# Kernel optimization log

Hardware: AMD Instinct MI355X
Metric: run time of the kernel (lower is better)

The kernel has to match this reference:

```python
import jax, jax.numpy as jnp
import numpy as np
from jax import lax

DIM, D_INNER, D_STATE, D_CONV, DT_RANK = 256, 512, 16, 4, 16
B_, H_, W_ = 4, 64, 64


def setup_inputs() -> dict:
    key = jax.random.key(0)
    ks = jax.random.split(key, 10)
    s = lambda k, shape, scale: (jax.random.normal(k, shape, dtype=jnp.float32) * scale)
    inp = {
        "x": s(ks[0], (B_, DIM, H_, W_), 1.0),
        "in_proj_w": s(ks[1], (2 * D_INNER, DIM), DIM ** -0.5),
        "conv_w": s(ks[2], (D_INNER, 1, D_CONV), D_CONV ** -0.5),
        "conv_b": s(ks[3], (D_INNER,), 0.02),
        "x_proj_w": s(ks[4], (DT_RANK + 2 * D_STATE, D_INNER), D_INNER ** -0.5),
        "dt_proj_w": s(ks[5], (D_INNER, DT_RANK), DT_RANK ** -0.5),
        "dt_proj_b": s(ks[6], (D_INNER,), 0.02),
        # A_log init: log(arange(1..d_state)) broadcast over channels (standard S4D-real init)
        "A_log": jnp.broadcast_to(jnp.log(jnp.arange(1, D_STATE + 1, dtype=jnp.float32)), (D_INNER, D_STATE)).copy(),
        "D": jnp.ones((D_INNER,), dtype=jnp.float32),
        "out_proj_w": s(ks[7], (DIM, D_INNER), D_INNER ** -0.5),
    }
    return inp


def _mamba_forward(x, in_proj_w, conv_w, conv_b, x_proj_w, dt_proj_w, dt_proj_b, A_log, D, out_proj_w):
    b, c, h, w = x.shape
    L = h * w
    xs = x.reshape(b, c, L).transpose(0, 2, 1)                      # [b, L, dim]

    xz = jnp.einsum('bld,ed->ble', xs, in_proj_w)                   # [b, L, 2*d_inner]
    u, res = jnp.split(xz, 2, axis=-1)                              # each [b, L, d_inner]

    # causal depthwise conv1d over sequence
    u_t = u.transpose(0, 2, 1)                                      # [b, d_inner, L]
    u_t = lax.conv_general_dilated(u_t, conv_w, window_strides=(1,),
                                   padding=[(D_CONV - 1, 0)],
                                   feature_group_count=D_INNER,
                                   dimension_numbers=('NCH', 'OIH', 'NCH'))
    u = jax.nn.silu(u_t.transpose(0, 2, 1) + conv_b)                # [b, L, d_inner]

    dbc = jnp.einsum('bld,ed->ble', u, x_proj_w)                    # [b, L, dt_rank+2n]
    dt, Bm, Cm = jnp.split(dbc, [DT_RANK, DT_RANK + D_STATE], axis=-1)
    delta = jax.nn.softplus(jnp.einsum('blr,dr->bld', dt, dt_proj_w) + dt_proj_b)  # [b,L,d_inner]

    A = -jnp.exp(A_log)                                             # [d_inner, n]
    deltaA = jnp.exp(jnp.einsum('bld,dn->bldn', delta, A))          # [b,L,d,n]
    deltaBu = jnp.einsum('bld,bln,bld->bldn', delta, Bm, u)         # [b,L,d,n]

    def step(state, inp):
        dA, dBu, c_t = inp                                          # [b,d,n],[b,d,n],[b,n]
        state = dA * state + dBu
        y = jnp.einsum('bdn,bn->bd', state, c_t)
        return state, y

    init = jnp.zeros((b, D_INNER, D_STATE), dtype=x.dtype)
    _, ys = lax.scan(step, init, (jnp.moveaxis(deltaA, 1, 0),
                                  jnp.moveaxis(deltaBu, 1, 0),
                                  jnp.moveaxis(Cm, 1, 0)))
    y = jnp.moveaxis(ys, 0, 1) + u * D                              # [b, L, d_inner]
    y = y * jax.nn.silu(res)
    out = jnp.einsum('ble,de->bld', y, out_proj_w)                  # [b, L, dim]
    return out.transpose(0, 2, 1).reshape(b, c, h, w)


def reference(x, in_proj_w, conv_w, conv_b, x_proj_w, dt_proj_w, dt_proj_b, A_log, D, out_proj_w):
    return _mamba_forward(x, in_proj_w, conv_w, conv_b, x_proj_w, dt_proj_w, dt_proj_b, A_log, D, out_proj_w)
```

## Files before the change

kernel.cpp:

```cpp
#include <hip/hip_runtime.h>
#include <math.h>


namespace {
constexpr int kB   = 4;
constexpr int kDim = 256;
constexpr int kL   = 4096;
constexpr int kDI  = 512;
constexpr int kN   = 16;
constexpr int kNC  = 128;
constexpr int kCS  = 32;
}

typedef __attribute__((ext_vector_type(8))) short bf16x8;
typedef __attribute__((ext_vector_type(4))) float f32x4;
typedef __attribute__((ext_vector_type(2))) float f32x2;

__device__ __forceinline__ float rcpf(float x) { return __builtin_amdgcn_rcpf(x); }
__device__ __forceinline__ float siluf(float x) { return x * rcpf(1.f + __expf(-x)); }
__device__ __forceinline__ float softplusf(float x) {
  return fmaxf(x, 0.f) + __logf(1.f + __expf(-fabsf(x)));
}

__device__ __forceinline__ unsigned short f2bf(float x) {
  union { float f; unsigned int u; } v; v.f = x;
  unsigned int u = v.u;
  u += 0x7fffu + ((u >> 16) & 1u);
  return (unsigned short)(u >> 16);
}
__device__ __forceinline__ float bf2f(unsigned short u) {
  union { unsigned int i; float f; } v; v.i = ((unsigned int)u) << 16; return v.f;
}

__device__ __forceinline__ void gload_lds16(const void* g, void* l) {
  __builtin_amdgcn_global_load_lds(
      (const __attribute__((address_space(1))) unsigned int*)g,
      (__attribute__((address_space(3))) unsigned int*)l, 16, 0, 0);
}

__global__ __launch_bounds__(256) void k_prep(const float* __restrict__ w_in,
                                              const float* __restrict__ w_out,
                                              const float* __restrict__ w_x,
                                              const float* __restrict__ w_dt,
                                              const float* __restrict__ A_log,
                                              const float* __restrict__ x,
                                              unsigned short* __restrict__ wib,
                                              unsigned short* __restrict__ wob,
                                              unsigned short* __restrict__ wxb,
                                              unsigned short* __restrict__ wdtb,
                                              float* __restrict__ Avz,
                                              unsigned int* __restrict__ flagA,
                                              unsigned short* __restrict__ xt) {
  __shared__ float Xs[64][65];
  const int blk = blockIdx.x;
  const int t = threadIdx.x;
  if (blk < 1760) {
    int idx = blk * 256 + t;
    if (idx < 262144) wib[idx] = f2bf(w_in[idx]);
    else if (idx < 393216) wob[idx - 262144] = f2bf(w_out[idx - 262144]);
    else if (idx < 417792) wxb[idx - 393216] = f2bf(w_x[idx - 393216]);
    else {
      int i = idx - 417792;
      int r = i & 31, d = i >> 5;
      wdtb[i] = (r < 16) ? f2bf(w_dt[d * 16 + r]) : (unsigned short)0;
    }
  } else if (blk < 1762) {
    int d = (blk - 1760) * 256 + t;
    float a0 = -__expf(A_log[d * kN]);
    bool ok = true;
#pragma unroll
    for (int n = 1; n < kN; ++n) {
      float av = -__expf(A_log[d * kN + n]);
      ok = ok && (fabsf(av - (n + 1) * a0) <= 1e-5f * fabsf(av));
    }
    Avz[d] = a0;
    unsigned long long bal = __ballot(ok);
    int wv = t >> 6;
    if ((t & 63) == 0) ((unsigned long long*)Xs)[wv] = bal;
    __syncthreads();
    if (t == 0) {
      unsigned long long all = ~0ull;
#pragma unroll
      for (int w = 0; w < 4; ++w) all &= ((unsigned long long*)Xs)[w];
      flagA[blk - 1760] = (all == ~0ull) ? 1u : 0u;
    }
  } else {
    int id = blk - 1762;
    int lb = id & 63, db = (id >> 6) & 3, b = id >> 8;
    const int d0 = db * 64, l0 = lb * 64, l = t & 63;
#pragma unroll
    for (int rep = 0; rep < 16; ++rep) {
      int dd = rep * 4 + (t >> 6);
      Xs[dd][l] = x[((size_t)b * kDim + d0 + dd) * kL + l0 + l];
    }
    __syncthreads();
#pragma unroll
    for (int rep = 0; rep < 8; ++rep) {
      int lj = rep * 8 + (t >> 5);
      int di = (t & 31) * 2;
      ushort2 v;
      v.x = f2bf(Xs[di][lj]);
      v.y = f2bf(Xs[di + 1][lj]);
      *(ushort2*)(xt + ((size_t)b * kL + l0 + lj) * kDim + d0 + di) = v;
    }
  }
}

__global__ __launch_bounds__(256) void gemm_in_lm(const unsigned short* __restrict__ xt,
                                                  const unsigned short* __restrict__ W,
                                                  unsigned short* __restrict__ ubf,
                                                  unsigned short* __restrict__ resb) {
  __shared__ __align__(16) unsigned short As[128 * 64];
  __shared__ __align__(16) unsigned short Bs[128 * 64];
  const int e0 = blockIdx.x * 128;
  const int l0 = blockIdx.y * 128;
  const int b  = blockIdx.z;
  const int t  = threadIdx.x;
  const int wave = t >> 6, lane = t & 63;
  const int wm = wave >> 1, wn = wave & 1;
  const unsigned short* Ab = xt + (size_t)b * kL * kDim;

  f32x4 acc[4][4];
#pragma unroll
  for (int i = 0; i < 4; ++i)
#pragma unroll
    for (int j = 0; j < 4; ++j) acc[i][j] = (f32x4)0.0f;

  const int srow = t >> 3, sch = t & 7;
  for (int kt = 0; kt < 4; ++kt) {
    const int k0 = kt * 64;
#pragma unroll
    for (int c = 0; c < 4; ++c) {
      int row = c * 32 + srow;
      int gch = sch ^ (row & 7);
      gload_lds16(Ab + (size_t)(l0 + row) * kDim + k0 + gch * 8,
                  (char*)As + c * 4096 + wave * 1024);
      gload_lds16(W  + (size_t)(e0 + row) * kDim + k0 + gch * 8,
                  (char*)Bs + c * 4096 + wave * 1024);
    }
    __syncthreads();
#pragma unroll
    for (int ks = 0; ks < 2; ++ks) {
      bf16x8 af[4], bfr[4];
#pragma unroll
      for (int f = 0; f < 4; ++f) {
        int ra = wm * 64 + f * 16 + (lane & 15);
        int ca = (ks * 4 + (lane >> 4)) ^ (ra & 7);
        af[f] = *(const bf16x8*)((const char*)As + ra * 128 + ca * 16);
        int rb = wn * 64 + f * 16 + (lane & 15);
        int cb = (ks * 4 + (lane >> 4)) ^ (rb & 7);
        bfr[f] = *(const bf16x8*)((const char*)Bs + rb * 128 + cb * 16);
      }
#pragma unroll
      for (int i = 0; i < 4; ++i)
#pragma unroll
        for (int j = 0; j < 4; ++j)
          acc[i][j] = __builtin_amdgcn_mfma_f32_16x16x32_bf16(af[i], bfr[j], acc[i][j], 0, 0, 0);
    }
    __syncthreads();
  }

  const bool is_u = (e0 < kDI);
  unsigned short* dst = is_u ? ubf : resb;
  const int ebase = is_u ? e0 : (e0 - kDI);
#pragma unroll
  for (int i = 0; i < 4; ++i)
#pragma unroll
    for (int j = 0; j < 4; ++j)
#pragma unroll
      for (int r = 0; r < 4; ++r) {
        int l = l0 + wm * 64 + i * 16 + (lane >> 4) * 4 + r;
        int e = ebase + wn * 64 + j * 16 + (lane & 15);
        dst[((size_t)b * kL + l) * kDI + e] = f2bf(acc[i][j][r]);
      }
}

__global__ __launch_bounds__(256) void k_conv(const unsigned short* __restrict__ ubf,
                                              const float* __restrict__ cw,
                                              const float* __restrict__ cb,
                                              unsigned short* __restrict__ ucb) {
  int idx = blockIdx.x * 256 + threadIdx.x;
  int d8 = idx & 63;
  int l  = (idx >> 6) & (kL - 1);
  int b  = idx >> 18;
  int d0 = d8 * 8;
  const unsigned short* row = ubf + ((size_t)b * kL + l) * kDI + d0;
  uint4 zero = make_uint4(0, 0, 0, 0);
  uint4 c0 = *(const uint4*)row;
  uint4 c1 = (l >= 1) ? *(const uint4*)(row - kDI)     : zero;
  uint4 c2 = (l >= 2) ? *(const uint4*)(row - 2 * kDI) : zero;
  uint4 c3 = (l >= 3) ? *(const uint4*)(row - 3 * kDI) : zero;
  const unsigned int* p0 = (const unsigned int*)&c0;
  const unsigned int* p1 = (const unsigned int*)&c1;
  const unsigned int* p2 = (const unsigned int*)&c2;
  const unsigned int* p3 = (const unsigned int*)&c3;
  unsigned short ov[8];
#pragma unroll
  for (int c = 0; c < 8; ++c) {
    int q = c >> 1, hi = c & 1;
    float u0 = bf2f((unsigned short)(hi ? (p0[q] >> 16) : (p0[q] & 0xffff)));
    float u1 = bf2f((unsigned short)(hi ? (p1[q] >> 16) : (p1[q] & 0xffff)));
    float u2 = bf2f((unsigned short)(hi ? (p2[q] >> 16) : (p2[q] & 0xffff)));
    float u3 = bf2f((unsigned short)(hi ? (p3[q] >> 16) : (p3[q] & 0xffff)));
    float4 w = *(const float4*)(cw + (d0 + c) * 4);
    float acc = cb[d0 + c] + w.x * u3 + w.y * u2 + w.z * u1 + w.w * u0;
    ov[c] = f2bf(siluf(acc));
  }
  *(uint4*)(ucb + ((size_t)b * kL + l) * kDI + d0) = *(const uint4*)ov;
}

__global__ __launch_bounds__(256) void k_xproj_dt(const unsigned short* __restrict__ Wx,
                                                  const unsigned short* __restrict__ Wdtb,
                                                  const float* __restrict__ bdt,
                                                  float* __restrict__ dbcBC,
                                                  const unsigned short* __restrict__ ucb,
                                                  unsigned short* __restrict__ delb) {
  __shared__ __align__(16) unsigned short As[64 * 64];
  __shared__ __align__(16) unsigned short Bs[128 * 64];
  __shared__ __align__(16) unsigned short dtTl[128 * 32];
  __shared__ __align__(16) unsigned short Wl[128 * 32];
  const int l0 = blockIdx.x * 128;
  const int b  = blockIdx.y;
  const int t  = threadIdx.x;
  const int wave = t >> 6, lane = t & 63;
  const unsigned short* Bb = ucb + (size_t)b * kL * kDI;

  f32x4 acc[3][2];
#pragma unroll
  for (int i = 0; i < 3; ++i)
#pragma unroll
    for (int j = 0; j < 2; ++j) acc[i][j] = (f32x4)0.0f;

  const int srow = t >> 3, sch = t & 7;
  for (int kt = 0; kt < 8; ++kt) {
    const int k0 = kt * 64;
#pragma unroll
    for (int c = 0; c < 2; ++c) {
      int row = c * 32 + srow;
      int grow = row < 48 ? row : 47;
      int gch = sch ^ (row & 7);
      gload_lds16(Wx + (size_t)grow * kDI + k0 + gch * 8,
                  (char*)As + c * 4096 + wave * 1024);
    }
#pragma unroll
    for (int c = 0; c < 4; ++c) {
      int row = c * 32 + srow;
      int gch = sch ^ (row & 7);
      gload_lds16(Bb + (size_t)(l0 + row) * kDI + k0 + gch * 8,
                  (char*)Bs + c * 4096 + wave * 1024);
    }
    __syncthreads();
#pragma unroll
    for (int ks = 0; ks < 2; ++ks) {
      bf16x8 af[3], bfr[2];
#pragma unroll
      for (int f = 0; f < 3; ++f) {
        int ra = f * 16 + (lane & 15);
        int ca = (ks * 4 + (lane >> 4)) ^ (ra & 7);
        af[f] = *(const bf16x8*)((const char*)As + ra * 128 + ca * 16);
      }
#pragma unroll
      for (int f = 0; f < 2; ++f) {
        int rb = wave * 32 + f * 16 + (lane & 15);
        int cb = (ks * 4 + (lane >> 4)) ^ (rb & 7);
        bfr[f] = *(const bf16x8*)((const char*)Bs + rb * 128 + cb * 16);
      }
#pragma unroll
      for (int i = 0; i < 3; ++i)
#pragma unroll
        for (int j = 0; j < 2; ++j)
          acc[i][j] = __builtin_amdgcn_mfma_f32_16x16x32_bf16(af[i], bfr[j], acc[i][j], 0, 0, 0);
    }
    __syncthreads();
  }

#pragma unroll
  for (int i = 1; i < 3; ++i)
#pragma unroll
    for (int j = 0; j < 2; ++j)
#pragma unroll
      for (int r = 0; r < 4; ++r) {
        int m = i * 16 + (lane >> 4) * 4 + r;
        int l = l0 + wave * 32 + j * 16 + (lane & 15);
        dbcBC[((size_t)b * 32 + (m - 16)) * kL + l] = acc[i][j][r];
      }
#pragma unroll
  for (int j = 0; j < 2; ++j) {
    int l = wave * 32 + j * 16 + (lane & 15);
    int m0 = (lane >> 4) * 4;
    ushort4 v;
    v.x = f2bf(acc[0][j][0]); v.y = f2bf(acc[0][j][1]);
    v.z = f2bf(acc[0][j][2]); v.w = f2bf(acc[0][j][3]);
    int byte = l * 64 + (((m0 >> 3) ^ (l & 3)) << 4) + ((m0 & 7) << 1);
    *(ushort4*)((char*)dtTl + byte) = v;
  }
  {
    int lz = t >> 1, zc = 2 + (t & 1);
    *(uint4*)((char*)dtTl + lz * 64 + ((zc ^ (lz & 3)) << 4)) = make_uint4(0, 0, 0, 0);
  }
  __syncthreads();

  const int wl = wave >> 1, wd = wave & 1;
  for (int dt4 = 0; dt4 < 4; ++dt4) {
#pragma unroll
    for (int c2 = 0; c2 < 2; ++c2) {
      int unit = c2 * 256 + t;
      int row = unit >> 2, sc = unit & 3;
      int gch = sc ^ (row & 3);
      gload_lds16(Wdtb + (size_t)(dt4 * 128 + row) * 32 + gch * 8,
                  (char*)Wl + c2 * 4096 + t * 16);
    }
    __syncthreads();
    f32x4 acc2[4][4];
#pragma unroll
    for (int i = 0; i < 4; ++i)
#pragma unroll
      for (int j = 0; j < 4; ++j) acc2[i][j] = (f32x4)0.0f;
    bf16x8 afr[4], bfr2[4];
#pragma unroll
    for (int f = 0; f < 4; ++f) {
      int ra = wl * 64 + f * 16 + (lane & 15);
      afr[f] = *(const bf16x8*)((const char*)dtTl + ra * 64 + (((lane >> 4) ^ (ra & 3)) << 4));
      int rb = wd * 64 + f * 16 + (lane & 15);
      bfr2[f] = *(const bf16x8*)((const char*)Wl + rb * 64 + (((lane >> 4) ^ (rb & 3)) << 4));
    }
#pragma unroll
    for (int i = 0; i < 4; ++i)
#pragma unroll
      for (int j = 0; j < 4; ++j)
        acc2[i][j] = __builtin_amdgcn_mfma_f32_16x16x32_bf16(afr[i], bfr2[j], acc2[i][j], 0, 0, 0);
#pragma unroll
    for (int j = 0; j < 4; ++j) {
      int d = dt4 * 128 + wd * 64 + j * 16 + (lane & 15);
      float bd = bdt[d];
#pragma unroll
      for (int i = 0; i < 4; ++i)
#pragma unroll
        for (int r = 0; r < 4; ++r) {
          int l = l0 + wl * 64 + i * 16 + (lane >> 4) * 4 + r;
          float delta = softplusf(acc2[i][j][r] + bd);
          delb[((size_t)b * kL + l) * kDI + d] = f2bf(delta);
        }
    }
    __syncthreads();
  }
}

__global__ __launch_bounds__(256) void k_scanA(const unsigned short* __restrict__ delb,
                                               const unsigned short* __restrict__ ucb,
                                               const float* __restrict__ dbcBC,
                                               const float* __restrict__ A_log,
                                               const float* __restrict__ Avz,
                                               const unsigned int* __restrict__ flagA,
                                               float* __restrict__ P,
                                               float* __restrict__ S) {
  __shared__ __align__(16) float Bsh[16][kCS];
  const int b = blockIdx.z, ch = blockIdx.y;
  const int t = threadIdx.x;
  const int d = blockIdx.x * 256 + t;
  const int l0 = ch * kCS;
  {
    int row = t >> 4, li = (t & 15) * 2;
    *(float2*)&Bsh[row][li] =
        *(const float2*)&dbcBC[((size_t)b * 32 + row) * kL + l0 + li];
  }
  __syncthreads();
  const bool fast = (flagA[0] != 0u) && (flagA[1] != 0u);
  const float Av0 = Avz[d];
  const unsigned short* pDel = delb + ((size_t)b * kL + l0) * kDI + d;
  const unsigned short* pU = ucb + ((size_t)b * kL + l0) * kDI + d;
  size_t obase = (size_t)(b * kNC + ch) * (kN * kDI) + d;

  if (fast) {
    f32x2 Sv2[8];
#pragma unroll
    for (int m = 0; m < 8; ++m) Sv2[m] = (f32x2){0.f, 0.f};
    float Pprod = 1.f;
    for (int i = 0; i < kCS; i += 4) {
      f32x2 a2[4], e2[4], du2[4];
#pragma unroll
      for (int jj = 0; jj < 4; ++jj) {
        float dl = bf2f(pDel[(size_t)(i + jj) * kDI]);
        float uu = bf2f(pU[(size_t)(i + jj) * kDI]);
        float E = __expf(dl * Av0);
        float duv = dl * uu;
        du2[jj] = (f32x2){duv, duv};
        float Esq = E * E;
        a2[jj] = (f32x2){E, Esq};
        e2[jj] = (f32x2){Esq, Esq};
        Pprod *= E;
      }
#pragma unroll
      for (int m = 0; m < 8; ++m) {
        float4 Ba = *(const float4*)&Bsh[2 * m][i];
        float4 Bb = *(const float4*)&Bsh[2 * m + 1][i];
        Sv2[m] = Sv2[m] * a2[0] + du2[0] * (f32x2){Ba.x, Bb.x};
        Sv2[m] = Sv2[m] * a2[1] + du2[1] * (f32x2){Ba.y, Bb.y};
        Sv2[m] = Sv2[m] * a2[2] + du2[2] * (f32x2){Ba.z, Bb.z};
        Sv2[m] = Sv2[m] * a2[3] + du2[3] * (f32x2){Ba.w, Bb.w};
        if (m < 7) {
          a2[0] *= e2[0]; a2[1] *= e2[1]; a2[2] *= e2[2]; a2[3] *= e2[3];
        }
      }
    }
    float pw = Pprod;
#pragma unroll
    for (int n = 0; n < kN; ++n) {
      P[obase + (size_t)n * kDI] = pw;
      S[obase + (size_t)n * kDI] = (n & 1) ? Sv2[n >> 1].y : Sv2[n >> 1].x;
      pw *= Pprod;
    }
  } else {
    float Av[16];
#pragma unroll
    for (int n = 0; n < kN; ++n) Av[n] = -__expf(A_log[d * kN + n]);
    float Pv[16], Sv[16];
#pragma unroll
    for (int n = 0; n < kN; ++n) { Pv[n] = 1.f; Sv[n] = 0.f; }
    for (int i = 0; i < kCS; i += 4) {
      float del[4], du[4];
#pragma unroll
      for (int jj = 0; jj < 4; ++jj) {
        del[jj] = bf2f(pDel[(size_t)(i + jj) * kDI]);
        du[jj] = del[jj] * bf2f(pU[(size_t)(i + jj) * kDI]);
      }
#pragma unroll
      for (int n = 0; n < kN; ++n) {
        float4 B4 = *(const float4*)&Bsh[n][i];
        float a;
        a = __expf(del[0] * Av[n]); Pv[n] *= a; Sv[n] = Sv[n] * a + du[0] * B4.x;
        a = __expf(del[1] * Av[n]); Pv[n] *= a; Sv[n] = Sv[n] * a + du[1] * B4.y;
        a = __expf(del[2] * Av[n]); Pv[n] *= a; Sv[n] = Sv[n] * a + du[2] * B4.z;
        a = __expf(del[3] * Av[n]); Pv[n] *= a; Sv[n] = Sv[n] * a + du[3] * B4.w;
      }
    }
#pragma unroll
    for (int n = 0; n < kN; ++n) {
      P[obase + (size_t)n * kDI] = Pv[n];
      S[obase + (size_t)n * kDI] = Sv[n];
    }
  }
}

__global__ __launch_bounds__(256) void k_scanB(const float* __restrict__ P,
                                               const float* __restrict__ S,
                                               float* __restrict__ init) {
  int idx = blockIdx.x * 256 + threadIdx.x;
  int b = idx >> 13, nd = idx & 8191;
  size_t base = (size_t)b * kNC * 8192 + nd;
  float carry = 0.f;
  for (int c0 = 0; c0 < kNC; c0 += 8) {
    float p[8], s[8];
#pragma unroll
    for (int j = 0; j < 8; ++j) {
      size_t o = base + (size_t)(c0 + j) * 8192;
      p[j] = P[o]; s[j] = S[o];
    }
#pragma unroll
    for (int j = 0; j < 8; ++j) {
      init[base + (size_t)(c0 + j) * 8192] = carry;
      carry = p[j] * carry + s[j];
    }
  }
}

__global__ __launch_bounds__(256) void k_scanC(const unsigned short* __restrict__ delb,
                                               const unsigned short* __restrict__ ucb,
                                               const float* __restrict__ dbcBC,
                                               const float* __restrict__ A_log,
                                               const float* __restrict__ Avz,
                                               const unsigned int* __restrict__ flagA,
                                               const float* __restrict__ init,
                                               const unsigned short* __restrict__ resb,
                                               const float* __restrict__ Dp,
                                               unsigned short* __restrict__ yt) {
  __shared__ __align__(16) float BCsh[32][kCS];
  const int b = blockIdx.z, ch = blockIdx.y;
  const int t = threadIdx.x;
  const int d = blockIdx.x * 256 + t;
  const int l0 = ch * kCS;
  {
    int row = t >> 3, li = (t & 7) * 4;
    *(float4*)&BCsh[row][li] =
        *(const float4*)&dbcBC[((size_t)b * 32 + row) * kL + l0 + li];
  }
  __syncthreads();
  const bool fast = (flagA[0] != 0u) && (flagA[1] != 0u);
  const float Av0 = Avz[d];
  const float Dv = Dp[d];
  const unsigned short* pDel = delb + ((size_t)b * kL + l0) * kDI + d;
  const unsigned short* pU = ucb + ((size_t)b * kL + l0) * kDI + d;
  const unsigned short* pR = resb + ((size_t)b * kL + l0) * kDI + d;
  unsigned short* pY = yt + ((size_t)b * kL + l0) * kDI + d;
  size_t ibase = (size_t)(b * kNC + ch) * (kN * kDI) + d;

  if (fast) {
    f32x2 s2[8];
#pragma unroll
    for (int m = 0; m < 8; ++m)
      s2[m] = (f32x2){init[ibase + (size_t)(2 * m) * kDI],
                      init[ibase + (size_t)(2 * m + 1) * kDI]};
    for (int i = 0; i < kCS; i += 4) {
      float uv[4];
      f32x2 a2[4], e2[4], du2[4], yacc2[4];
#pragma unroll
      for (int jj = 0; jj < 4; ++jj) {
        float dl = bf2f(pDel[(size_t)(i + jj) * kDI]);
        uv[jj] = bf2f(pU[(size_t)(i + jj) * kDI]);
        float E = __expf(dl * Av0);
        float duv = dl * uv[jj];
        du2[jj] = (f32x2){duv, duv};
        float Esq = E * E;
        a2[jj] = (f32x2){E, Esq};
        e2[jj] = (f32x2){Esq, Esq};
        yacc2[jj] = (f32x2){0.f, 0.f};
      }
#pragma unroll
      for (int m = 0; m < 8; ++m) {
        float4 Ba = *(const float4*)&BCsh[2 * m][i];
        float4 Bb = *(const float4*)&BCsh[2 * m + 1][i];
        float4 Ca = *(const float4*)&BCsh[16 + 2 * m][i];
        float4 Cb = *(const float4*)&BCsh[16 + 2 * m + 1][i];
        s2[m] = s2[m] * a2[0] + du2[0] * (f32x2){Ba.x, Bb.x};
        yacc2[0] = yacc2[0] + s2[m] * (f32x2){Ca.x, Cb.x};
        s2[m] = s2[m] * a2[1] + du2[1] * (f32x2){Ba.y, Bb.y};
        yacc2[1] = yacc2[1] + s2[m] * (f32x2){Ca.y, Cb.y};
        s2[m] = s2[m] * a2[2] + du2[2] * (f32x2){Ba.z, Bb.z};
        yacc2[2] = yacc2[2] + s2[m] * (f32x2){Ca.z, Cb.z};
        s2[m] = s2[m] * a2[3] + du2[3] * (f32x2){Ba.w, Bb.w};
        yacc2[3] = yacc2[3] + s2[m] * (f32x2){Ca.w, Cb.w};
        if (m < 7) {
          a2[0] *= e2[0]; a2[1] *= e2[1]; a2[2] *= e2[2]; a2[3] *= e2[3];
        }
      }
#pragma unroll
      for (int jj = 0; jj < 4; ++jj) {
        float yv = yacc2[jj].x + yacc2[jj].y;
        float r = bf2f(pR[(size_t)(i + jj) * kDI]);
        float gv = (yv + uv[jj] * Dv) * siluf(r);
        pY[(size_t)(i + jj) * kDI] = f2bf(gv);
      }
    }
  } else {
    float Av[16];
#pragma unroll
    for (int n = 0; n < kN; ++n) Av[n] = -__expf(A_log[d * kN + n]);
    float s[16];
#pragma unroll
    for (int n = 0; n < kN; ++n) s[n] = init[ibase + (size_t)n * kDI];
    for (int i = 0; i < kCS; i += 4) {
      float uv[4], du[4], del[4], yacc[4] = {0.f, 0.f, 0.f, 0.f};
#pragma unroll
      for (int jj = 0; jj < 4; ++jj) {
        del[jj] = bf2f(pDel[(size_t)(i + jj) * kDI]);
        uv[jj] = bf2f(pU[(size_t)(i + jj) * kDI]);
        du[jj] = del[jj] * uv[jj];
      }
#pragma unroll
      for (int n = 0; n < kN; ++n) {
        float4 B4 = *(const float4*)&BCsh[n][i];
        float4 C4 = *(const float4*)&BCsh[16 + n][i];
        float a;
        a = __expf(del[0] * Av[n]); s[n] = s[n] * a + du[0] * B4.x; yacc[0] += s[n] * C4.x;
        a = __expf(del[1] * Av[n]); s[n] = s[n] * a + du[1] * B4.y; yacc[1] += s[n] * C4.y;
        a = __expf(del[2] * Av[n]); s[n] = s[n] * a + du[2] * B4.z; yacc[2] += s[n] * C4.z;
        a = __expf(del[3] * Av[n]); s[n] = s[n] * a + du[3] * B4.w; yacc[3] += s[n] * C4.w;
      }
#pragma unroll
      for (int jj = 0; jj < 4; ++jj) {
        float r = bf2f(pR[(size_t)(i + jj) * kDI]);
        float gv = (yacc[jj] + uv[jj] * Dv) * siluf(r);
        pY[(size_t)(i + jj) * kDI] = f2bf(gv);
      }
    }
  }
}

__global__ __launch_bounds__(256) void gemm_out(const unsigned short* __restrict__ A,
                                                const unsigned short* __restrict__ Bt,
                                                float* __restrict__ C0) {
  __shared__ __align__(16) unsigned short As[128 * 64];
  __shared__ __align__(16) unsigned short Bs[128 * 64];
  const int n0 = blockIdx.x * 128;
  const int m0 = blockIdx.y * 128;
  const int b  = blockIdx.z;
  const int t  = threadIdx.x;
  const int wave = t >> 6, lane = t & 63;
  const int wm = wave >> 1, wn = wave & 1;
  const unsigned short* Bb = Bt + (size_t)b * kL * kDI;

  f32x4 acc[4][4];
#pragma unroll
  for (int i = 0; i < 4; ++i)
#pragma unroll
    for (int j = 0; j < 4; ++j) acc[i][j] = (f32x4)0.0f;

  const int srow = t >> 3, sch = t & 7;
  for (int kt = 0; kt < 8; ++kt) {
    const int k0 = kt * 64;
#pragma unroll
    for (int c = 0; c < 4; ++c) {
      int row = c * 32 + srow;
      int gch = sch ^ (row & 7);
      gload_lds16(A  + (size_t)(m0 + row) * kDI + k0 + gch * 8,
                  (char*)As + c * 4096 + wave * 1024);
      gload_lds16(Bb + (size_t)(n0 + row) * kDI + k0 + gch * 8,
                  (char*)Bs + c * 4096 + wave * 1024);
    }
    __syncthreads();
#pragma unroll
    for (int ks = 0; ks < 2; ++ks) {
      bf16x8 af[4], bfr[4];
#pragma unroll
      for (int f = 0; f < 4; ++f) {
        int ra = wm * 64 + f * 16 + (lane & 15);
        int ca = (ks * 4 + (lane >> 4)) ^ (ra & 7);
        af[f] = *(const bf16x8*)((const char*)As + ra * 128 + ca * 16);
        int rb = wn * 64 + f * 16 + (lane & 15);
        int cb = (ks * 4 + (lane >> 4)) ^ (rb & 7);
        bfr[f] = *(const bf16x8*)((const char*)Bs + rb * 128 + cb * 16);
      }
#pragma unroll
      for (int i = 0; i < 4; ++i)
#pragma unroll
        for (int j = 0; j < 4; ++j)
          acc[i][j] = __builtin_amdgcn_mfma_f32_16x16x32_bf16(af[i], bfr[j], acc[i][j], 0, 0, 0);
    }
    __syncthreads();
  }
#pragma unroll
  for (int i = 0; i < 4; ++i)
#pragma unroll
    for (int j = 0; j < 4; ++j)
#pragma unroll
      for (int r = 0; r < 4; ++r) {
        int m = m0 + wm * 64 + i * 16 + (lane >> 4) * 4 + r;
        int n = n0 + wn * 64 + j * 16 + (lane & 15);
        C0[((size_t)b * kDim + m) * kL + n] = acc[i][j][r];
      }
}

extern "C" void kernel_launch(void* const* d_in, const int* in_sizes, int n_in,
                              void* d_out, int out_size, void* d_ws, size_t ws_size,
                              hipStream_t stream) {
  const float* x       = (const float*)d_in[0];
  const float* in_w    = (const float*)d_in[1];
  const float* conv_w  = (const float*)d_in[2];
  const float* conv_b  = (const float*)d_in[3];
  const float* xproj_w = (const float*)d_in[4];
  const float* dt_w    = (const float*)d_in[5];
  const float* dt_b    = (const float*)d_in[6];
  const float* A_log   = (const float*)d_in[7];
  const float* Dp      = (const float*)d_in[8];
  const float* out_w   = (const float*)d_in[9];
  float* out = (float*)d_out;

  float* ws = (float*)d_ws;
  const size_t nBLD  = (size_t)kB * kL * kDI;
  const size_t nPS   = (size_t)kB * kNC * kN * kDI;
  float* dbcBC = ws;
  float* Pb    = dbcBC + 524288;
  float* Sb    = Pb + nPS;
  float* initb = Sb + nPS;
  unsigned short* ubf  = (unsigned short*)(initb + nPS);
  unsigned short* ucb  = ubf + nBLD;
  unsigned short* resb = ucb + nBLD;
  unsigned short* delb = resb + nBLD;
  unsigned short* wib  = delb + nBLD;
  unsigned short* wob  = wib + 262144;
  unsigned short* wxb  = wob + 131072;
  unsigned short* wdtb = wxb + 24576;
  float* Avz           = (float*)(wdtb + 32768);
  unsigned int* flagA  = (unsigned int*)(Avz + 512);
  unsigned short* xt   = delb;
  unsigned short* yt   = (unsigned short*)Pb;

  k_prep<<<dim3(2786), 256, 0, stream>>>(in_w, out_w, xproj_w, dt_w, A_log, x,
                                         wib, wob, wxb, wdtb, Avz, flagA, xt);
  gemm_in_lm<<<dim3(8, kL / 128, kB), 256, 0, stream>>>(xt, wib, ubf, resb);
  k_conv<<<dim3((unsigned)(kB * kL * 64 / 256)), 256, 0, stream>>>(ubf, conv_w, conv_b, ucb);
  k_xproj_dt<<<dim3(kL / 128, kB), 256, 0, stream>>>(wxb, wdtb, dt_b, dbcBC, ucb, delb);
  k_scanA<<<dim3(2, kNC, kB), 256, 0, stream>>>(delb, ucb, dbcBC, A_log, Avz, flagA, Pb, Sb);
  k_scanB<<<dim3(kB * kDI * kN / 256), 256, 0, stream>>>(Pb, Sb, initb);
  k_scanC<<<dim3(2, kNC, kB), 256, 0, stream>>>(delb, ucb, dbcBC, A_log, Avz, flagA, initb, resb, Dp, yt);
  gemm_out<<<dim3(kL / 128, kDim / 128, kB), 256, 0, stream>>>(wob, yt, out);
}
```

Measured before the change: 155.0 us.

## Store per-chunk decay product once and rebuild state powers in scanB

```diff
diff --git a/kernel.cpp b/kernel.cpp
--- a/kernel.cpp
+++ b/kernel.cpp
@@ -346,23 +346,24 @@
   }
 }
 
-__global__ __launch_bounds__(256) void k_scanA(const unsigned short* __restrict__ delb,
+__global__ __launch_bounds__(128) void k_scanA(const unsigned short* __restrict__ delb,
                                                const unsigned short* __restrict__ ucb,
                                                const float* __restrict__ dbcBC,
                                                const float* __restrict__ A_log,
                                                const float* __restrict__ Avz,
                                                const unsigned int* __restrict__ flagA,
-                                               float* __restrict__ P,
+                                               float* __restrict__ Pprod,
+                                               float* __restrict__ Pfull,
                                                float* __restrict__ S) {
   __shared__ __align__(16) float Bsh[16][kCS];
   const int b = blockIdx.z, ch = blockIdx.y;
   const int t = threadIdx.x;
-  const int d = blockIdx.x * 256 + t;
+  const int d = blockIdx.x * 128 + t;
   const int l0 = ch * kCS;
   {
-    int row = t >> 4, li = (t & 15) * 2;
-    *(float2*)&Bsh[row][li] =
-        *(const float2*)&dbcBC[((size_t)b * 32 + row) * kL + l0 + li];
+    int row = t >> 3, li = (t & 7) * 4;
+    *(float4*)&Bsh[row][li] =
+        *(const float4*)&dbcBC[((size_t)b * 32 + row) * kL + l0 + li];
   }
   __syncthreads();
   const bool fast = (flagA[0] != 0u) && (flagA[1] != 0u);
@@ -375,7 +376,7 @@
     f32x2 Sv2[8];
 #pragma unroll
     for (int m = 0; m < 8; ++m) Sv2[m] = (f32x2){0.f, 0.f};
-    float Pprod = 1.f;
+    float Pp = 1.f;
     for (int i = 0; i < kCS; i += 4) {
       f32x2 a2[4], e2[4], du2[4];
 #pragma unroll
@@ -388,7 +389,7 @@
         float Esq = E * E;
         a2[jj] = (f32x2){E, Esq};
         e2[jj] = (f32x2){Esq, Esq};
-        Pprod *= E;
+        Pp *= E;
       }
 #pragma unroll
       for (int m = 0; m < 8; ++m) {
@@ -403,13 +404,10 @@
         }
       }
     }
-    float pw = Pprod;
-#pragma unroll
-    for (int n = 0; n < kN; ++n) {
-      P[obase + (size_t)n * kDI] = pw;
+    Pprod[(size_t)(b * kNC + ch) * kDI + d] = Pp;
+#pragma unroll
+    for (int n = 0; n < kN; ++n)
       S[obase + (size_t)n * kDI] = (n & 1) ? Sv2[n >> 1].y : Sv2[n >> 1].x;
-      pw *= Pprod;
-    }
   } else {
     float Av[16];
 #pragma unroll
@@ -436,35 +434,65 @@
     }
 #pragma unroll
     for (int n = 0; n < kN; ++n) {
-      P[obase + (size_t)n * kDI] = Pv[n];
+      Pfull[obase + (size_t)n * kDI] = Pv[n];
       S[obase + (size_t)n * kDI] = Sv[n];
     }
   }
 }
 
-__global__ __launch_bounds__(256) void k_scanB(const float* __restrict__ P,
+__global__ __launch_bounds__(256) void k_scanB(const float* __restrict__ Pprod,
+                                               const float* __restrict__ Pfull,
                                                const float* __restrict__ S,
+                                               const unsigned int* __restrict__ flagA,
                                                float* __restrict__ init) {
   int idx = blockIdx.x * 256 + threadIdx.x;
   int b = idx >> 13, nd = idx & 8191;
+  int n = nd >> 9, d = nd & 511;
   size_t base = (size_t)b * kNC * 8192 + nd;
+  const bool fast = (flagA[0] != 0u) && (flagA[1] != 0u);
   float carry = 0.f;
-  for (int c0 = 0; c0 < kNC; c0 += 8) {
-    float p[8], s[8];
-#pragma unroll
-    for (int j = 0; j < 8; ++j) {
-      size_t o = base + (size_t)(c0 + j) * 8192;
-      p[j] = P[o]; s[j] = S[o];
-    }
-#pragma unroll
-    for (int j = 0; j < 8; ++j) {
-      init[base + (size_t)(c0 + j) * 8192] = carry;
-      carry = p[j] * carry + s[j];
-    }
-  }
-}
-
-__global__ __launch_bounds__(256) void k_scanC(const unsigned short* __restrict__ delb,
+  if (fast) {
+    size_t pbase = (size_t)b * kNC * kDI + d;
+    const int e = n + 1;
+    for (int c0 = 0; c0 < kNC; c0 += 8) {
+      float p[8], s[8];
+#pragma unroll
+      for (int j = 0; j < 8; ++j) {
+        float pr = Pprod[pbase + (size_t)(c0 + j) * kDI];
+        float p2 = pr * pr, p4 = p2 * p2, p8 = p4 * p4;
+        float pw = 1.f;
+        if (e & 1) pw *= pr;
+        if (e & 2) pw *= p2;
+        if (e & 4) pw *= p4;
+        if (e & 8) pw *= p8;
+        if (e & 16) pw *= p8 * p8;
+        p[j] = pw;
+        s[j] = S[base + (size_t)(c0 + j) * 8192];
+      }
+#pragma unroll
+      for (int j = 0; j < 8; ++j) {
+        init[base + (size_t)(c0 + j) * 8192] = carry;
+        carry = p[j] * carry + s[j];
+      }
+    }
+  } else {
+    for (int c0 = 0; c0 < kNC; c0 += 8) {
+      float p[8], s[8];
+#pragma unroll
+      for (int j = 0; j < 8; ++j) {
+        size_t o = base + (size_t)(c0 + j) * 8192;
+        p[j] = Pfull[o]; s[j] = S[o];
+      }
+#pragma unroll
+      for (int j = 0; j < 8; ++j) {
+        init[base + (size_t)(c0 + j) * 8192] = carry;
+        carry = p[j] * carry + s[j];
+      }
+    }
+  }
+}
+
+__global__ __launch_bounds__(128) void k_scanC(const unsigned short* __restrict__ delb,
                                                const unsigned short* __restrict__ ucb,
                                                const float* __restrict__ dbcBC,
                                                const float* __restrict__ A_log,
@@ -477,12 +505,14 @@
   __shared__ __align__(16) float BCsh[32][kCS];
   const int b = blockIdx.z, ch = blockIdx.y;
   const int t = threadIdx.x;
-  const int d = blockIdx.x * 256 + t;
+  const int d = blockIdx.x * 128 + t;
   const int l0 = ch * kCS;
   {
-    int row = t >> 3, li = (t & 7) * 4;
+    int row = t >> 2, li = (t & 3) * 8;
     *(float4*)&BCsh[row][li] =
         *(const float4*)&dbcBC[((size_t)b * 32 + row) * kL + l0 + li];
+    *(float4*)&BCsh[row][li + 4] =
+        *(const float4*)&dbcBC[((size_t)b * 32 + row) * kL + l0 + li + 4];
   }
   __syncthreads();
   const bool fast = (flagA[0] != 0u) && (flagA[1] != 0u);
@@ -658,11 +688,11 @@
   float* ws = (float*)d_ws;
   const size_t nBLD  = (size_t)kB * kL * kDI;
   const size_t nPS   = (size_t)kB * kNC * kN * kDI;
-  float* dbcBC = ws;
-  float* Pb    = dbcBC + 524288;
-  float* Sb    = Pb + nPS;
-  float* initb = Sb + nPS;
-  unsigned short* ubf  = (unsigned short*)(initb + nPS);
+  float* dbcBC  = ws;
+  float* Sb     = dbcBC + 524288;
+  float* initb  = Sb + nPS;
+  float* Pprodb = initb + nPS;
+  unsigned short* ubf  = (unsigned short*)(Pprodb + 262144);
   unsigned short* ucb  = ubf + nBLD;
   unsigned short* resb = ucb + nBLD;
   unsigned short* delb = resb + nBLD;
@@ -673,15 +703,16 @@
   float* Avz           = (float*)(wdtb + 32768);
   unsigned int* flagA  = (unsigned int*)(Avz + 512);
   unsigned short* xt   = delb;
-  unsigned short* yt   = (unsigned short*)Pb;
+  float* Pfull         = (float*)ubf;
+  unsigned short* yt   = (unsigned short*)Sb;
 
   k_prep<<<dim3(2786), 256, 0, stream>>>(in_w, out_w, xproj_w, dt_w, A_log, x,
                                          wib, wob, wxb, wdtb, Avz, flagA, xt);
   gemm_in_lm<<<dim3(8, kL / 128, kB), 256, 0, stream>>>(xt, wib, ubf, resb);
   k_conv<<<dim3((unsigned)(kB * kL * 64 / 256)), 256, 0, stream>>>(ubf, conv_w, conv_b, ucb);
   k_xproj_dt<<<dim3(kL / 128, kB), 256, 0, stream>>>(wxb, wdtb, dt_b, dbcBC, ucb, delb);
-  k_scanA<<<dim3(2, kNC, kB), 256, 0, stream>>>(delb, ucb, dbcBC, A_log, Avz, flagA, Pb, Sb);
-  k_scanB<<<dim3(kB * kDI * kN / 256), 256, 0, stream>>>(Pb, Sb, initb);
-  k_scanC<<<dim3(2, kNC, kB), 256, 0, stream>>>(delb, ucb, dbcBC, A_log, Avz, flagA, initb, resb, Dp, yt);
+  k_scanA<<<dim3(4, kNC, kB), 128, 0, stream>>>(delb, ucb, dbcBC, A_log, Avz, flagA, Pprodb, Pfull, Sb);
+  k_scanB<<<dim3(kB * kDI * kN / 256), 256, 0, stream>>>(Pprodb, Pfull, Sb, flagA, initb);
+  k_scanC<<<dim3(4, kNC, kB), 128, 0, stream>>>(delb, ucb, dbcBC, A_log, Avz, flagA, initb, resb, Dp, yt);
   gemm_out<<<dim3(kL / 128, kDim / 128, kB), 256, 0, stream>>>(wob, yt, out);
 }
```

Result: no change. 156.3 us (+0.8%).
